# Performance work log

Measured on AMD Instinct MI355X. Metric: run time of the kernel, lower is better.

The kernel has to match this reference:

```python
import jax, jax.numpy as jnp
import numpy as np


def setup_inputs() -> dict:
    key = jax.random.key(0)
    k1, k2, k3 = jax.random.split(key, 3)
    B, C, H, Wd, p = 64, 3, 448, 448, 28
    x = jax.random.normal(k1, (B, C, H, Wd), dtype=jnp.float32)
    W = jax.random.normal(k2, (3, 3, p, p), dtype=jnp.float32) * 0.02
    b = jax.random.normal(k3, (3,), dtype=jnp.float32) * 0.02
    return {"x": x, "W": W, "b": b, "patch_size": p}


def reference(x, W, b, patch_size):
    # Conv2d(3->3, kernel=stride=patch_size) == blockwise contraction over each patch.
    B, C, H, Wd = x.shape
    p = patch_size
    Hp, Wp = H // p, Wd // p
    N = Hp * Wp
    # [B, C, Hp, p, Wp, p]
    xr = x.reshape(B, C, Hp, p, Wp, p)
    # patches: [B, 3(out), Hp, Wp]
    patches = jnp.einsum('bchiwj,ocij->bohw', xr, W) + b[None, :, None, None]
    # Bilinear upsample of a 1x1 map is a constant broadcast; mean over channels
    # commutes with the broadcast, so compute channel-mean first then broadcast.
    m = patches.mean(axis=1)  # [B, Hp, Wp]
    out = jnp.broadcast_to(m.reshape(B, N, 1, 1), (B, N, p, p))
    return out
```

## Files before the change

kernel.cpp:

```cpp
#include <hip/hip_runtime.h>


typedef float f32x4 __attribute__((ext_vector_type(4)));

#define WS_M_OFF 2560

__global__ __launch_bounds__(256) void k0_prep(
    const float* __restrict__ W, const float* __restrict__ bias,
    float* __restrict__ ws) {
  const int t = threadIdx.x;
  const float4* W4 = reinterpret_cast<const float4*>(W);
  float4* o = reinterpret_cast<float4*>(ws);
  for (int f = t; f < 588; f += 256) {
    const float4 a = W4[f], g = W4[f + 588], h = W4[f + 1176];
    o[f] = make_float4((a.x + g.x + h.x) * (1.f / 3.f),
                       (a.y + g.y + h.y) * (1.f / 3.f),
                       (a.z + g.z + h.z) * (1.f / 3.f),
                       (a.w + g.w + h.w) * (1.f / 3.f));
  }
  if (t == 0) ws[2352] = (bias[0] + bias[1] + bias[2]) * (1.f / 3.f);
}

__global__ __launch_bounds__(256) void k1_reduce(
    const float* __restrict__ x, const float* __restrict__ ws_w,
    float* __restrict__ ws_m) {
  const int t    = threadIdx.x;
  const int lane = t & 63;
  const int P    = blockIdx.x * 4 + (t >> 6);
  const int b    = P >> 8;
  const int rem  = P & 255;
  const int hp   = rem >> 4;
  const int wp   = rem & 15;

  const char* xbase = reinterpret_cast<const char*>(
      x + (size_t)b * 602112 + (size_t)hp * 12544 + wp * 28);
  const float4* wm4 = reinterpret_cast<const float4*>(ws_w);

  float s = 0.f;
  #pragma unroll
  for (int it = 0; it < 9; ++it) {
    const int f  = it * 64 + lane;
    const int c  = (f * 1339) >> 18;
    const int r2 = f - c * 196;
    const int i  = (r2 * 9363) >> 16;
    const int j4 = r2 - i * 7;
    const float4 v = *reinterpret_cast<const float4*>(
        xbase + c * 802816 + i * 1792 + j4 * 16);
    const float4 w = wm4[f];
    s += v.x * w.x + v.y * w.y + v.z * w.z + v.w * w.w;
  }
  {
    const int f = 576 + lane;
    if (f < 588) {
      const int c  = (f * 1339) >> 18;
      const int r2 = f - c * 196;
      const int i  = (r2 * 9363) >> 16;
      const int j4 = r2 - i * 7;
      const float4 v = *reinterpret_cast<const float4*>(
          xbase + c * 802816 + i * 1792 + j4 * 16);
      const float4 w = wm4[f];
      s += v.x * w.x + v.y * w.y + v.z * w.z + v.w * w.w;
    }
  }
  #pragma unroll
  for (int m = 32; m >= 1; m >>= 1) s += __shfl_xor(s, m, 64);
  if (lane == 0) ws_m[P] = s + ws_w[2352];
}

__global__ __launch_bounds__(256) void k2_write(
    const float* __restrict__ ws_m, float* __restrict__ out) {
  const int t    = threadIdx.x;
  const int lane = t & 63;
  const int P    = blockIdx.x * 4 + (t >> 6);
  const float s  = ws_m[P];
  f32x4* o4 = reinterpret_cast<f32x4*>(out + (size_t)P * 784);
  const f32x4 val = {s, s, s, s};
  #pragma unroll
  for (int it = 0; it < 4; ++it) {
    const int idx = it * 64 + lane;
    if (idx < 196) o4[idx] = val;
  }
}

extern "C" void kernel_launch(void* const* d_in, const int* in_sizes, int n_in,
                              void* d_out, int out_size, void* d_ws, size_t ws_size,
                              hipStream_t stream) {
  const float* x    = (const float*)d_in[0];
  const float* W    = (const float*)d_in[1];
  const float* bias = (const float*)d_in[2];
  float* out = (float*)d_out;
  float* ws  = (float*)d_ws;
  k0_prep <<<dim3(1),    dim3(256), 0, stream>>>(W, bias, ws);
  k1_reduce<<<dim3(4096), dim3(256), 0, stream>>>(x, ws, ws + WS_M_OFF);
  k2_write <<<dim3(4096), dim3(256), 0, stream>>>(ws + WS_M_OFF, out);
}
```

Baseline: 242.8 us.

## Fuse weight prep, patch reduction and broadcast write into one kernel

Merges the three kernels into a single launch. Each block now averages the weights across output channels into shared memory, computes the patch dot product, adds the averaged bias, and writes the broadcast output directly with nontemporal stores. This removes two launches and the workspace round trip for the weights and per-patch means. In exchange, every block redoes the weight averaging and pays a barrier before it starts.

```diff
diff --git a/kernel.cpp b/kernel.cpp
--- a/kernel.cpp
+++ b/kernel.cpp
@@ -3,38 +3,35 @@
 
 typedef float f32x4 __attribute__((ext_vector_type(4)));
 
-#define WS_M_OFF 2560
+__global__ __launch_bounds__(256) void patchify_kernel(
+    const float* __restrict__ x, const float* __restrict__ W,
+    const float* __restrict__ bias, float* __restrict__ out) {
+  __shared__ float4 sW4[588];
 
-__global__ __launch_bounds__(256) void k0_prep(
-    const float* __restrict__ W, const float* __restrict__ bias,
-    float* __restrict__ ws) {
-  const int t = threadIdx.x;
-  const float4* W4 = reinterpret_cast<const float4*>(W);
-  float4* o = reinterpret_cast<float4*>(ws);
-  for (int f = t; f < 588; f += 256) {
-    const float4 a = W4[f], g = W4[f + 588], h = W4[f + 1176];
-    o[f] = make_float4((a.x + g.x + h.x) * (1.f / 3.f),
-                       (a.y + g.y + h.y) * (1.f / 3.f),
-                       (a.z + g.z + h.z) * (1.f / 3.f),
-                       (a.w + g.w + h.w) * (1.f / 3.f));
-  }
-  if (t == 0) ws[2352] = (bias[0] + bias[1] + bias[2]) * (1.f / 3.f);
-}
-
-__global__ __launch_bounds__(256) void k1_reduce(
-    const float* __restrict__ x, const float* __restrict__ ws_w,
-    float* __restrict__ ws_m) {
   const int t    = threadIdx.x;
   const int lane = t & 63;
-  const int P    = blockIdx.x * 4 + (t >> 6);
-  const int b    = P >> 8;
-  const int rem  = P & 255;
-  const int hp   = rem >> 4;
-  const int wp   = rem & 15;
+
+  if (t < 256) {
+    for (int f = t; f < 588; f += 256) {
+      const float4 a = reinterpret_cast<const float4*>(W)[f];
+      const float4 g = reinterpret_cast<const float4*>(W)[f + 588];
+      const float4 h = reinterpret_cast<const float4*>(W)[f + 1176];
+      sW4[f] = make_float4((a.x + g.x + h.x) * (1.f / 3.f),
+                           (a.y + g.y + h.y) * (1.f / 3.f),
+                           (a.z + g.z + h.z) * (1.f / 3.f),
+                           (a.w + g.w + h.w) * (1.f / 3.f));
+    }
+  }
+  __syncthreads();
+
+  const int P   = blockIdx.x * 4 + (t >> 6);
+  const int b   = P >> 8;
+  const int rem = P & 255;
+  const int hp  = rem >> 4;
+  const int wp  = rem & 15;
 
   const char* xbase = reinterpret_cast<const char*>(
       x + (size_t)b * 602112 + (size_t)hp * 12544 + wp * 28);
-  const float4* wm4 = reinterpret_cast<const float4*>(ws_w);
 
   float s = 0.f;
   #pragma unroll
@@ -46,7 +43,7 @@
     const int j4 = r2 - i * 7;
     const float4 v = *reinterpret_cast<const float4*>(
         xbase + c * 802816 + i * 1792 + j4 * 16);
-    const float4 w = wm4[f];
+    const float4 w = sW4[f];
     s += v.x * w.x + v.y * w.y + v.z * w.z + v.w * w.w;
   }
   {
@@ -58,27 +55,21 @@
       const int j4 = r2 - i * 7;
       const float4 v = *reinterpret_cast<const float4*>(
           xbase + c * 802816 + i * 1792 + j4 * 16);
-      const float4 w = wm4[f];
+      const float4 w = sW4[f];
       s += v.x * w.x + v.y * w.y + v.z * w.z + v.w * w.w;
     }
   }
+
   #pragma unroll
   for (int m = 32; m >= 1; m >>= 1) s += __shfl_xor(s, m, 64);
-  if (lane == 0) ws_m[P] = s + ws_w[2352];
-}
+  s += (bias[0] + bias[1] + bias[2]) * (1.f / 3.f);
 
-__global__ __launch_bounds__(256) void k2_write(
-    const float* __restrict__ ws_m, float* __restrict__ out) {
-  const int t    = threadIdx.x;
-  const int lane = t & 63;
-  const int P    = blockIdx.x * 4 + (t >> 6);
-  const float s  = ws_m[P];
   f32x4* o4 = reinterpret_cast<f32x4*>(out + (size_t)P * 784);
   const f32x4 val = {s, s, s, s};
   #pragma unroll
   for (int it = 0; it < 4; ++it) {
     const int idx = it * 64 + lane;
-    if (idx < 196) o4[idx] = val;
+    if (idx < 196) __builtin_nontemporal_store(val, o4 + idx);
   }
 }
 
@@ -89,8 +80,5 @@
   const float* W    = (const float*)d_in[1];
   const float* bias = (const float*)d_in[2];
   float* out = (float*)d_out;
-  float* ws  = (float*)d_ws;
-  k0_prep <<<dim3(1),    dim3(256), 0, stream>>>(W, bias, ws);
-  k1_reduce<<<dim3(4096), dim3(256), 0, stream>>>(x, ws, ws + WS_M_OFF);
-  k2_write <<<dim3(4096), dim3(256), 0, stream>>>(ws + WS_M_OFF, out);
+  patchify_kernel<<<dim3(4096), dim3(256), 0, stream>>>(x, W, bias, out);
 }
```

Result: faster. 235.8 us (-2.9%).
